# Optimization experiments

Measured on AMD Instinct MI355X. Metric: run time of the kernel, lower is better.

The kernel has to match this reference:

```python
import jax, jax.numpy as jnp
import numpy as np

NS, NV, NB, L = 64, 32, 8, 4      # scalar channels, vector channels, bessel bases, layers
EMB = 32                           # atom-type embedding dim
MAX_R = 3.0                        # cutoff radius
NUM_NEIGH = 32.0                   # avg degree used for scatter normalization
N, E = 10000, 320000
NW = NS * 2 + NV * 2               # per-edge tensor-product weights from radial MLP
MAX_TYPES = 10


def smooth_cutoff(x):
    # e3nn md-example smooth_cutoff: 1 for x<0.5, 0 for x>1, cosine blend between
    u = 2.0 * (x - 1.0)
    y = (1.0 - jnp.cos(jnp.pi * u)) * 0.5
    y = jnp.where(u > 0.0, 0.0, y)
    y = jnp.where(u < -1.0, 1.0, y)
    return y


def bessel_basis(r):
    # soft_one_hot_linspace(basis='bessel', cutoff=False) * sqrt(NB)
    n = jnp.arange(1, NB + 1, dtype=r.dtype)
    y = jnp.sqrt(2.0 / MAX_R) * jnp.sin(n * jnp.pi * r[:, None] / MAX_R) / r[:, None]
    return y * np.sqrt(NB).astype(np.float32)


def edge_info(x, src, dst):
    feats, attrs = [], []
    for i in range(2):  # nvec = x.shape[-1] // 3 = 2
        vec = x[src, 3 * i:3 * i + 3] - x[dst, 3 * i:3 * i + 3]  # [E,3]
        r = jnp.linalg.norm(vec, axis=1)
        sh = np.float32(np.sqrt(3.0)) * vec / r[:, None]          # 1x1o SH, component norm
        feats.append(bessel_basis(r))
        attrs.append(smooth_cutoff(r / MAX_R)[:, None] * sh)
    return jnp.concatenate(feats, axis=-1), jnp.stack(attrs, axis=1)  # [E,2*NB], [E,2,3]


def _forward(x, emb_table, W_up, W_proj, fc1, b1, fc2, W_sv, W_vs, W_sc_s, W_sc_v, Ws, Wv, h, mix, node_attr, edge_src, edge_dst):
    n = x.shape[0]
    inv_nb = np.float32(1.0 / np.sqrt(NUM_NEIGH))
    # uplift: 2 input vectors -> NV hidden vectors, NS hidden scalars (zero init)
    xv = x.reshape(n, 2, 3)
    v = jnp.einsum('nic,iv->nvc', xv, W_up)        # [n,NV,3]
    s = jnp.zeros((n, NS), x.dtype)                # [n,NS]
    s_old, v_old = s, v
    attr_emb = emb_table[node_attr]                # [n,EMB]
    xcur = x
    for i in range(L):
        f, a = edge_info(xcur, edge_src, edge_dst)            # [E,2NB], [E,2,3]
        w = jax.nn.silu(f @ fc1[i] + b1[i]) @ fc2[i]          # [E,NW] radial TP weights
        w1 = w[:, :NS * 2].reshape(-1, NS, 2)                 # 0e x 1o -> 1o path weights
        w2 = w[:, NS * 2:].reshape(-1, NV, 2)                 # 1o x 1o -> 0e path weights
        # equivariant tensor-product messages (gather at edge_src)
        t = s[edge_src][:, :, None] * w1                      # [E,NS,2]
        q = jnp.einsum('euv,uvm->evm', t, W_sv[i])            # [E,2,NV]
        msg_v = jnp.einsum('evm,evc->emc', q, a)              # [E,NV,3]
        d = jnp.einsum('euc,evc->euv', v[edge_src], a)        # [E,NV,2]
        msg_s = jnp.einsum('euv,uvm->em', d * w2, W_vs[i])    # [E,NS+NV]
        # scatter-add at edge_dst, normalized by sqrt(num_neighbors)
        agg_s = jnp.zeros((n, NS + NV), x.dtype).at[edge_dst].add(msg_s) * inv_nb
        agg_v = jnp.zeros((n, NV, 3), x.dtype).at[edge_dst].add(msg_v) * inv_nb
        # self-connection: fully-connected TP with node-attr scalars
        sc_s = jnp.einsum('nu,ne,uem->nm', s, attr_emb, W_sc_s[i])
        sc_v = jnp.einsum('nuc,ne,uev->nvc', v, attr_emb, W_sc_v[i])
        cs = sc_s + agg_s
        cv = sc_v + agg_v
        # Gate: silu on scalars, sigmoid gate scalars modulate vectors
        gs = jax.nn.silu(cs[:, :NS])
        gate = jax.nn.sigmoid(cs[:, NS:])
        gv = cv * gate[:, :, None]
        # self-interaction (equivariant linear per degree)
        si_s = s @ Ws[i]
        si_v = jnp.einsum('nuc,uv->nvc', v, Wv[i])
        # verlet-like update
        hi2 = h[i] ** 2
        s_new = 2.0 * s - s_old + hi2 * (mix[i] * gs + (mix[i] - 1.0) * si_s)
        v_new = 2.0 * v - v_old + hi2 * (mix[i] * gv + (mix[i] - 1.0) * si_v)
        s_old, v_old = s, v
        s, v = s_new, v_new
        # project back to x for next layer's edge features
        xcur = jnp.einsum('nvc,vi->nic', v, W_proj).reshape(n, 6)
    return xcur


def setup_inputs() -> dict:
    key = jax.random.key(0)
    ks = jax.random.split(key, 20)
    x = jax.random.normal(ks[0], (N, 6), jnp.float32)
    node_attr = jax.random.randint(ks[1], (N,), 0, MAX_TYPES)
    edge_src = jax.random.randint(ks[2], (E,), 0, N)
    off = jax.random.randint(ks[3], (E,), 1, N)
    edge_dst = (edge_src + off) % N  # no self-loops -> no zero edge_vec
    batch = jnp.zeros((N,), jnp.int32)
    rn = lambda k, sh, sc: jax.random.normal(k, sh, jnp.float32) * np.float32(sc)
    emb_table = rn(ks[4], (MAX_TYPES, EMB), 0.5)
    W_up = rn(ks[5], (2, NV), 1.0 / np.sqrt(2))
    W_proj = rn(ks[6], (NV, 2), 1.0 / np.sqrt(NV))
    fc1 = rn(ks[7], (L, 2 * NB, 64), 1.0 / np.sqrt(2 * NB))
    b1 = jnp.zeros((L, 64), jnp.float32)
    fc2 = rn(ks[8], (L, 64, NW), 1.0 / np.sqrt(64))
    W_sv = rn(ks[9], (L, NS, 2, NV), 1.0 / np.sqrt(NS * 2))
    W_vs = rn(ks[10], (L, NV, 2, NS + NV), 1.0 / np.sqrt(NV * 2))
    W_sc_s = rn(ks[11], (L, NS, EMB, NS + NV), 1.0 / np.sqrt(NS * EMB))
    W_sc_v = rn(ks[12], (L, NV, EMB, NV), 1.0 / np.sqrt(NV * EMB))
    Ws = rn(ks[13], (L, NS, NS), 1.0 / np.sqrt(NS))
    Wv = rn(ks[14], (L, NV, NV), 1.0 / np.sqrt(NV))
    h = jnp.ones((L,), jnp.float32) * 0.01
    mix = jnp.ones((L,), jnp.float32) * 0.5
    return {"x": x, "emb_table": emb_table, "W_up": W_up, "W_proj": W_proj, "fc1": fc1, "b1": b1, "fc2": fc2, "W_sv": W_sv, "W_vs": W_vs, "W_sc_s": W_sc_s, "W_sc_v": W_sc_v, "Ws": Ws, "Wv": Wv, "h": h, "mix": mix, "node_attr": node_attr, "edge_src": edge_src, "edge_dst": edge_dst, "batch": batch}


def reference(x, emb_table, W_up, W_proj, fc1, b1, fc2, W_sv, W_vs, W_sc_s, W_sc_v, Ws, Wv, h, mix, node_attr, edge_src, edge_dst, batch):
    return _forward(x, emb_table, W_up, W_proj, fc1, b1, fc2, W_sv, W_vs, W_sc_s, W_sc_v, Ws, Wv, h, mix, node_attr, edge_src, edge_dst)
```

## Files before the change

### kernel.cpp

```cpp
#include <hip/hip_runtime.h>
#include <math.h>

constexpr int cNS = 64, cNV = 32, cNB = 8, cL = 4, cEMB = 32, cNT = 10;
constexpr float PI_F = 3.14159265358979323846f;
constexpr float INV_SQRT_NN = 0.17677669529663687f;
constexpr float BESSEL_C = 2.3094010767585034f;
constexpr float SQRT3 = 1.7320508075688772f;

typedef unsigned short u16;
typedef unsigned int u32;
typedef unsigned long long u64;
typedef __attribute__((ext_vector_type(8))) short bf16x8;
typedef __attribute__((ext_vector_type(4))) float f32x4;
typedef __attribute__((ext_vector_type(2))) float f32x2;
typedef __attribute__((ext_vector_type(4))) int i32x4;

__device__ __forceinline__ u16 f2b(float x) {
  u32 u = __float_as_uint(x);
  return (u16)((u + 0x7fffu + ((u >> 16) & 1u)) >> 16);
}
__device__ __forceinline__ float b2f(u16 h) { return __uint_as_float(((u32)h) << 16); }
__device__ __forceinline__ float blo(u32 w) { return __uint_as_float(w << 16); }
__device__ __forceinline__ float bhi(u32 w) { return __uint_as_float(w & 0xffff0000u); }

__device__ __forceinline__ u32 pkbf(float lo, float hi) {
  u32 r;
  asm("v_cvt_pk_bf16_f32 %0, %1, %2" : "=v"(r) : "v"(lo), "v"(hi));
  return r;
}

__device__ __forceinline__ void lds_fence() {
  asm volatile("s_waitcnt lgkmcnt(0)" ::: "memory");
  __builtin_amdgcn_sched_barrier(0);
}

union U8 { bf16x8 v; u32 w[4]; };

__device__ __forceinline__ f32x4 mfma16(bf16x8 a, bf16x8 b, f32x4 c) {
  return __builtin_amdgcn_mfma_f32_16x16x32_bf16(a, b, c, 0, 0, 0);
}


__global__ void k_precompA(const float* __restrict__ emb, const float* __restrict__ Wss,
                           float* __restrict__ A) {
  int idx = blockIdx.x * 256 + threadIdx.x;
  if (idx >= cL * cNT * 64 * 96) return;
  int m = idx % 96;
  int u = (idx / 96) % 64;
  int t = (idx / (96 * 64)) % cNT;
  int l = idx / (96 * 64 * cNT);
  float acc = 0.f;
#pragma unroll
  for (int e = 0; e < 32; ++e)
    acc += emb[t * 32 + e] * Wss[((size_t)(l * 64 + u) * 32 + e) * 96 + m];
  A[idx] = acc;
}

__global__ void k_precompB(const float* __restrict__ emb, const float* __restrict__ Wsv_,
                           float* __restrict__ B) {
  int idx = blockIdx.x * 256 + threadIdx.x;
  if (idx >= cL * cNT * 32 * 32) return;
  int vo = idx % 32;
  int u = (idx / 32) % 32;
  int t = (idx / 1024) % cNT;
  int l = idx / (1024 * cNT);
  float acc = 0.f;
#pragma unroll
  for (int e = 0; e < 32; ++e)
    acc += emb[t * 32 + e] * Wsv_[((size_t)(l * 32 + u) * 32 + e) * 32 + vo];
  B[idx] = acc;
}

__global__ void k_packB(const float* __restrict__ fc2, const float* __restrict__ Wsv,
                        const float* __restrict__ Wvs, const float* __restrict__ fc1,
                        u16* __restrict__ fc2L, u16* __restrict__ WsvL,
                        u16* __restrict__ WvsL, u16* __restrict__ fc1L) {
  int idx = blockIdx.x * 256 + threadIdx.x;
  const int T1 = cL * 12288, T2 = cL * 2 * 2048, T3 = cL * 2 * 3072, T4 = cL * 2048;
  if (idx < T1) {
    int l = idx / 12288, r = idx % 12288;
    int ki = r & 7, tt = r >> 3;
    int nn = tt % 192, kq = tt / 192;
    fc2L[idx] = f2b(fc2[((size_t)(l * 64) + kq * 8 + ki) * 192 + nn]);
  } else if (idx < T1 + T2) {
    int r0 = idx - T1;
    int l = r0 / 4096, r1 = r0 % 4096;
    int k2 = r1 / 2048, r = r1 % 2048;
    int ki = r & 7, tt = r >> 3;
    int mm = tt % 32, kq = tt / 32;
    WsvL[r0] = f2b(Wsv[((size_t)((l * 64 + kq * 8 + ki) * 2) + k2) * 32 + mm]);
  } else if (idx < T1 + T2 + T3) {
    int r0 = idx - T1 - T2;
    int l = r0 / 6144, r1 = r0 % 6144;
    int k2 = r1 / 3072, r = r1 % 3072;
    int ki = r & 7, tt = r >> 3;
    int mm = tt % 96, kq = tt / 96;
    WvsL[r0] = f2b(Wvs[((size_t)((l * 32 + kq * 8 + ki) * 2) + k2) * 96 + mm]);
  } else if (idx < T1 + T2 + T3 + T4) {
    int r0 = idx - T1 - T2 - T3;
    int l = r0 / 2048, r1 = r0 % 2048;
    int kq = r1 / 512, rem = r1 % 512;
    int n = rem / 8, ki = rem & 7;
    fc1L[r0] = (kq < 2) ? f2b(fc1[l * 1024 + (kq * 8 + ki) * 64 + n]) : (u16)0;
  }
}

__global__ void k_init(const float* __restrict__ x, const float* __restrict__ Wup,
                       float* __restrict__ v, float* __restrict__ v_old,
                       float* __restrict__ xcur, int N) {
  int idx = blockIdx.x * 256 + threadIdx.x;
  if (idx >= N * 32) return;
  int n = idx >> 5, vc = idx & 31;
  float w0 = Wup[vc], w1 = Wup[32 + vc];
#pragma unroll
  for (int c = 0; c < 3; ++c) {
    float val = x[n * 6 + c] * w0 + x[n * 6 + 3 + c] * w1;
    v[idx * 3 + c] = val;
    v_old[idx * 3 + c] = val;
  }
  if (vc < 6) xcur[n * 6 + vc] = x[n * 6 + vc];
}


__global__ void k_zero_i(int* __restrict__ p, int n) {
  int i = blockIdx.x * 256 + threadIdx.x;
  if (i < n) p[i] = 0;
}

__global__ void k_hist(const int* __restrict__ edst, int* __restrict__ deg, int E) {
  int e = blockIdx.x * 256 + threadIdx.x;
  if (e < E) atomicAdd(&deg[edst[e]], 1);
}

__global__ __launch_bounds__(1024) void k_scan(const int* __restrict__ deg,
                                               int* __restrict__ row_ptr,
                                               int* __restrict__ cursor, int N) {
  __shared__ int part[1024];
  int t = threadIdx.x;
  int chunk = (N + 1023) / 1024;
  int base = t * chunk;
  int sum = 0;
  for (int i = 0; i < chunk; ++i) {
    int idx = base + i;
    if (idx < N) sum += deg[idx];
  }
  part[t] = sum;
  __syncthreads();
  for (int off = 1; off < 1024; off <<= 1) {
    int val = (t >= off) ? part[t - off] : 0;
    __syncthreads();
    part[t] += val;
    __syncthreads();
  }
  int run = (t > 0) ? part[t - 1] : 0;
  for (int i = 0; i < chunk; ++i) {
    int idx = base + i;
    if (idx < N) {
      row_ptr[idx] = run;
      cursor[idx] = run;
      run += deg[idx];
    }
  }
  if (t == 1023) row_ptr[N] = part[1023];
}

__global__ void k_scatter(const int* __restrict__ esrc, const int* __restrict__ edst,
                          int* __restrict__ cursor, int* __restrict__ esrc_s,
                          int* __restrict__ edst_s, int E) {
  int e = blockIdx.x * 256 + threadIdx.x;
  if (e < E) {
    int d = edst[e];
    int p = atomicAdd(&cursor[d], 1);
    esrc_s[p] = esrc[e];
    edst_s[p] = d;
  }
}

template <bool SZERO>
__global__ __launch_bounds__(256) void k_edge_mfma(
    const float* __restrict__ xcur, const float* __restrict__ s, const float* __restrict__ v,
    const int* __restrict__ esrc_s, const int* __restrict__ edst_s,
    const u16* __restrict__ fc1L, const float* __restrict__ b1,
    const u16* __restrict__ fc2L, const u16* __restrict__ WsvL0,
    const u16* __restrict__ WsvL1, const u16* __restrict__ WvsL0,
    const u16* __restrict__ WvsL1, u16* __restrict__ msgbuf, int E) {
  __shared__ u16 wbAll[4][16 * 200];
  __shared__ float aAll[4][16][6];
  int wid = threadIdx.x >> 6, lane = threadIdx.x & 63;
  int e0 = (blockIdx.x * 4 + wid) * 16;
  if (e0 >= E) return;
  u16* wb = wbAll[wid];
  int lrow = lane & 15, lg = lane >> 4;

  int prow = e0 + lrow;
  if (prow >= E) prow = E - 1;
  int src = esrc_s[prow];

  {
    int el = lane >> 2, qq = lane & 3;
    int ge = e0 + el;
    if (ge >= E) ge = E - 1;
    int gs = esrc_s[ge], gd = edst_s[ge];
    float xs[6], xd[6];
    {
      const float2* ps = (const float2*)(xcur + (size_t)gs * 6);
      const float2* pd = (const float2*)(xcur + (size_t)gd * 6);
      float2 A0 = ps[0], A1 = ps[1], A2 = ps[2];
      float2 B0 = pd[0], B1 = pd[1], B2 = pd[2];
      xs[0] = A0.x; xs[1] = A0.y; xs[2] = A1.x; xs[3] = A1.y; xs[4] = A2.x; xs[5] = A2.y;
      xd[0] = B0.x; xd[1] = B0.y; xd[2] = B1.x; xd[3] = B1.y; xd[4] = B2.x; xd[5] = B2.y;
    }
    float f[16], av[6];
#pragma unroll
    for (int i = 0; i < 2; ++i) {
      float vx = xs[3 * i + 0] - xd[3 * i + 0];
      float vy = xs[3 * i + 1] - xd[3 * i + 1];
      float vz = xs[3 * i + 2] - xd[3 * i + 2];
      float r2 = vx * vx + vy * vy + vz * vz;
      float rr = sqrtf(r2);
      float invr = 1.0f / rr;
      float th = (PI_F / 3.0f) * rr;
      float s1, c1;
      __sincosf(th, &s1, &c1);
      float twc = 2.0f * c1;
      float snm = 0.f, sn = s1;
      float fc = BESSEL_C * invr;
#pragma unroll
      for (int nn = 0; nn < 8; ++nn) {
        f[8 * i + nn] = fc * sn;
        float nx = twc * sn - snm;
        snm = sn;
        sn = nx;
      }
      float uu = (2.0f / 3.0f) * rr - 2.0f;
      float cut;
      if (uu > 0.f) cut = 0.f;
      else if (uu < -1.f) cut = 1.f;
      else cut = (1.0f - __cosf(PI_F * uu)) * 0.5f;
      float sc = cut * SQRT3 * invr;
      av[3 * i + 0] = vx * sc; av[3 * i + 1] = vy * sc; av[3 * i + 2] = vz * sc;
    }
    if (qq == 0) {
      u32* fp = (u32*)(wb + 1600 + el * 40);
#pragma unroll
      for (int i = 0; i < 8; ++i) fp[i] = pkbf(f[2 * i], f[2 * i + 1]);
#pragma unroll
      for (int i = 8; i < 16; ++i) fp[i] = 0u;
      float* ap = aAll[wid][el];
#pragma unroll
      for (int i = 0; i < 6; ++i) ap[i] = av[i];
    }
  }

  float sv0[8], sv1[8], vl[24];
  if (!SZERO) {
    const float* sp = s + (size_t)src * 64;
    *(f32x4*)(sv0) = *(const f32x4*)(sp + lg * 8);
    *(f32x4*)(sv0 + 4) = *(const f32x4*)(sp + lg * 8 + 4);
    *(f32x4*)(sv1) = *(const f32x4*)(sp + 32 + lg * 8);
    *(f32x4*)(sv1 + 4) = *(const f32x4*)(sp + 32 + lg * 8 + 4);
  }
  {
    const float* vp = v + (size_t)src * 96 + lg * 24;
#pragma unroll
    for (int i = 0; i < 6; ++i) *(f32x4*)(vl + 4 * i) = *(const f32x4*)(vp + 4 * i);
  }

  lds_fence();

  {
    bf16x8 fA = *(const bf16x8*)(wb + 1600 + lrow * 40 + lg * 8);
    f32x4 hp[4];
#pragma unroll
    for (int nb = 0; nb < 4; ++nb) {
      bf16x8 bB = *(const bf16x8*)(fc1L + (size_t)(lg * 64 + nb * 16 + lrow) * 8);
      f32x4 z = {0.f, 0.f, 0.f, 0.f};
      hp[nb] = mfma16(fA, bB, z);
    }
#pragma unroll
    for (int nb = 0; nb < 4; ++nb) {
      float bias = b1[nb * 16 + lrow];
      float hv[4];
#pragma unroll
      for (int r = 0; r < 4; ++r) {
        float xv = hp[nb][r] + bias;
        hv[r] = xv * (1.0f / (1.0f + __expf(-xv)));
      }
      u32 p01 = pkbf(hv[0], hv[1]);
      u32 p23 = pkbf(hv[2], hv[3]);
      int col = nb * 16 + lrow;
      wb[(4 * lg + 0) * 72 + col] = (u16)p01;
      wb[(4 * lg + 1) * 72 + col] = (u16)(p01 >> 16);
      wb[(4 * lg + 2) * 72 + col] = (u16)p23;
      wb[(4 * lg + 3) * 72 + col] = (u16)(p23 >> 16);
    }
  }
  lds_fence();

  bf16x8 ha = *(const bf16x8*)(wb + lrow * 72 + lg * 8);
  bf16x8 hbf = *(const bf16x8*)(wb + lrow * 72 + 32 + lg * 8);
  lds_fence();

  int xw = lg << 3;
#pragma unroll
  for (int nb = (SZERO ? 8 : 0); nb < 12; ++nb) {
    bf16x8 b0 = *(const bf16x8*)(fc2L + (size_t)(lg * 192 + nb * 16 + lrow) * 8);
    bf16x8 b1v = *(const bf16x8*)(fc2L + (size_t)((4 + lg) * 192 + nb * 16 + lrow) * 8);
    f32x4 c = {0.f, 0.f, 0.f, 0.f};
    c = mfma16(ha, b0, c);
    c = mfma16(hbf, b1v, c);
    int n = nb * 16 + lrow;
    int pn = (n < 128) ? ((n & 1) * 64 + (n >> 1)) : (128 + (n & 1) * 32 + ((n - 128) >> 1));
    int rbase = 4 * lg * 200 + (pn ^ xw);
    u32 p01 = pkbf(c[0], c[1]);
    u32 p23 = pkbf(c[2], c[3]);
    wb[rbase] = (u16)p01;
    wb[rbase + 200] = (u16)(p01 >> 16);
    wb[rbase + 400] = (u16)p23;
    wb[rbase + 600] = (u16)(p23 >> 16);
  }
  lds_fence();

  const u16* wrow = wb + lrow * 200 + (((lg ^ (lrow >> 2)) & 3) << 3);

  f32x4 q0[2], q1[2];
  if (!SZERO) {
    i32x4 W0a = *(const i32x4*)(wrow);
    i32x4 W0b = *(const i32x4*)(wrow + 32);
    i32x4 W1a = *(const i32x4*)(wrow + 64);
    i32x4 W1b = *(const i32x4*)(wrow + 96);
    U8 t0a, t0b, t1a, t1b;
#pragma unroll
    for (int j2 = 0; j2 < 4; ++j2) {
      u32 wa = (u32)W0a[j2], wbv = (u32)W0b[j2], wc = (u32)W1a[j2], wd = (u32)W1b[j2];
      t0a.w[j2] = pkbf(sv0[2 * j2] * blo(wa), sv0[2 * j2 + 1] * bhi(wa));
      t0b.w[j2] = pkbf(sv1[2 * j2] * blo(wbv), sv1[2 * j2 + 1] * bhi(wbv));
      t1a.w[j2] = pkbf(sv0[2 * j2] * blo(wc), sv0[2 * j2 + 1] * bhi(wc));
      t1b.w[j2] = pkbf(sv1[2 * j2] * blo(wd), sv1[2 * j2 + 1] * bhi(wd));
    }
#pragma unroll
    for (int nb = 0; nb < 2; ++nb) {
      bf16x8 bA = *(const bf16x8*)(WsvL0 + (size_t)(lg * 32 + nb * 16 + lrow) * 8);
      bf16x8 bB = *(const bf16x8*)(WsvL0 + (size_t)((4 + lg) * 32 + nb * 16 + lrow) * 8);
      f32x4 c = {0.f, 0.f, 0.f, 0.f};
      c = mfma16(t0a.v, bA, c);
      c = mfma16(t0b.v, bB, c);
      q0[nb] = c;
      bf16x8 bC = *(const bf16x8*)(WsvL1 + (size_t)(lg * 32 + nb * 16 + lrow) * 8);
      bf16x8 bD = *(const bf16x8*)(WsvL1 + (size_t)((4 + lg) * 32 + nb * 16 + lrow) * 8);
      f32x4 c2 = {0.f, 0.f, 0.f, 0.f};
      c2 = mfma16(t1a.v, bC, c2);
      c2 = mfma16(t1b.v, bD, c2);
      q1[nb] = c2;
    }
  }

  float a00, a01, a02, a10, a11, a12;
  {
    const float* ap = aAll[wid][lrow];
    a00 = ap[0]; a01 = ap[1]; a02 = ap[2]; a10 = ap[3]; a11 = ap[4]; a12 = ap[5];
  }
  i32x4 W2a = *(const i32x4*)(wrow + 128);
  i32x4 W2b = *(const i32x4*)(wrow + 160);
  U8 ga, gb;
#pragma unroll
  for (int j2 = 0; j2 < 4; ++j2) {
    float d0a, d1a, d0b, d1b;
    {
      float vx = vl[6 * j2 + 0], vy = vl[6 * j2 + 1], vz = vl[6 * j2 + 2];
      d0a = vx * a00 + vy * a01 + vz * a02;
      d1a = vx * a10 + vy * a11 + vz * a12;
    }
    {
      float vx = vl[6 * j2 + 3], vy = vl[6 * j2 + 4], vz = vl[6 * j2 + 5];
      d0b = vx * a00 + vy * a01 + vz * a02;
      d1b = vx * a10 + vy * a11 + vz * a12;
    }
    u32 wa = (u32)W2a[j2], wbv = (u32)W2b[j2];
    ga.w[j2] = pkbf(d0a * blo(wa), d0b * bhi(wa));
    gb.w[j2] = pkbf(d1a * blo(wbv), d1b * bhi(wbv));
  }
  f32x4 mS[6];
#pragma unroll
  for (int nb = 0; nb < 6; ++nb) {
    bf16x8 b0 = *(const bf16x8*)(WvsL0 + (size_t)(lg * 96 + nb * 16 + lrow) * 8);
    bf16x8 b1v = *(const bf16x8*)(WvsL1 + (size_t)(lg * 96 + nb * 16 + lrow) * 8);
    f32x4 c = {0.f, 0.f, 0.f, 0.f};
    c = mfma16(ga.v, b0, c);
    c = mfma16(gb.v, b1v, c);
    mS[nb] = c;
  }

  lds_fence();
#pragma unroll
  for (int nb = 0; nb < 6; ++nb) {
    u32 p01 = pkbf(mS[nb][0], mS[nb][1]);
    u32 p23 = pkbf(mS[nb][2], mS[nb][3]);
    int colx = (nb * 16 + lrow) ^ xw;
    wb[(4 * lg + 0) * 200 + colx] = (u16)p01;
    wb[(4 * lg + 1) * 200 + colx] = (u16)(p01 >> 16);
    wb[(4 * lg + 2) * 200 + colx] = (u16)p23;
    wb[(4 * lg + 3) * 200 + colx] = (u16)(p23 >> 16);
  }
  if (!SZERO) {
#pragma unroll
    for (int nb = 0; nb < 2; ++nb) {
#pragma unroll
      for (int r = 0; r < 4; ++r) {
        int el = 4 * lg + r;
        const float* ap = aAll[wid][el];
        float Q0v = q0[nb][r], Q1v = q1[nb][r];
        float v0 = Q0v * ap[0] + Q1v * ap[3];
        float v1 = Q0v * ap[1] + Q1v * ap[4];
        float v2 = Q0v * ap[2] + Q1v * ap[5];
        u32 p01 = pkbf(v0, v1);
        int base = el * 200 + ((96 + nb * 16 + lrow) ^ xw);
        wb[base] = (u16)p01;
        wb[base + 32] = (u16)(p01 >> 16);
        wb[base + 64] = f2b(v2);
      }
    }
  }
  lds_fence();

  int orow = lane >> 2, oq = lane & 3;
  if (e0 + orow < E) {
    const int OST = SZERO ? 96 : 192;
    u16* gdst = msgbuf + (size_t)(e0 + orow) * OST;
    int xo = ((orow >> 2) & 3) << 3;
    const int NIT = SZERO ? 3 : 6;
#pragma unroll
    for (int it = 0; it < NIT; ++it) {
      int col = oq * 8 + it * 32;
      i32x4 d = *(const i32x4*)(wb + orow * 200 + (col ^ xo));
      *(i32x4*)(gdst + col) = d;
    }
  }
}

template <bool SZERO>
__global__ __launch_bounds__(256) void k_gnode(
    const u16* __restrict__ msg, const int* __restrict__ row_ptr,
    float* __restrict__ s, float* __restrict__ sold, float* __restrict__ v,
    float* __restrict__ vold,
    const float* __restrict__ Amat, const float* __restrict__ Bmat,
    const float* __restrict__ Ws, const float* __restrict__ Wv,
    const float* __restrict__ Wproj, const int* __restrict__ nattr,
    const float* __restrict__ hArr, const float* __restrict__ mixArr, int layer,
    float* __restrict__ xout, int N) {
  int half = threadIdx.x >> 7;
  int t = threadIdx.x & 127;
  int n = blockIdx.x * 2 + half;
  bool active = n < N;
  if (!active) n = N - 1;
  __shared__ float agg[2][192];
  __shared__ float srow[2][64];
  __shared__ float vrow[2][96];
  __shared__ float gateS[2][32];
  __shared__ float vnewS[2][96];
  int start = row_ptr[n], end = row_ptr[n + 1];
  const int STRIDE = SZERO ? 96 : 192;
  int nacc4 = SZERO ? 24 : 48;
  if (t < nacc4) {
    const u16* mp = msg + (size_t)t * 4;
    float accA[4] = {0.f, 0.f, 0.f, 0.f};
    float accB[4] = {0.f, 0.f, 0.f, 0.f};
    int p = start;
    for (; p + 8 <= end; p += 8) {
      u64 w[8];
#pragma unroll
      for (int k = 0; k < 8; ++k) w[k] = *(const u64*)(mp + (size_t)(p + k) * STRIDE);
#pragma unroll
      for (int k = 0; k < 8; ++k) {
        u32 wl = (u32)w[k], wh = (u32)(w[k] >> 32);
        float* acc = (k & 1) ? accB : accA;
        acc[0] += blo(wl);
        acc[1] += bhi(wl);
        acc[2] += blo(wh);
        acc[3] += bhi(wh);
      }
    }
    for (; p < end; ++p) {
      u64 w = *(const u64*)(mp + (size_t)p * STRIDE);
      u32 wl = (u32)w, wh = (u32)(w >> 32);
      accA[0] += blo(wl);
      accA[1] += bhi(wl);
      accA[2] += blo(wh);
      accA[3] += bhi(wh);
    }
#pragma unroll
    for (int c = 0; c < 4; ++c)
      agg[half][4 * t + c] = (accA[c] + accB[c]) * INV_SQRT_NN;
  }
  if (SZERO && t >= 24 && t < 48) {
#pragma unroll
    for (int c = 0; c < 4; ++c) agg[half][4 * t + c] = 0.f;
  }
  if (t < 64) srow[half][t] = s[(size_t)n * 64 + t];
  if (t < 96) vrow[half][t] = v[(size_t)n * 96 + t];
  __syncthreads();
  int type = nattr[n];
  float hv = hArr[layer];
  float h2v = hv * hv;
  float mx = mixArr[layer];
  float cs = 0.f;
  if (t < 96) {
    cs = agg[half][t];
    const float* Ac = Amat + (size_t)type * 64 * 96 + t;
#pragma unroll 8
    for (int u = 0; u < 64; ++u) cs += srow[half][u] * Ac[u * 96];
  }
  if (t >= 64 && t < 96) gateS[half][t - 64] = 1.0f / (1.0f + __expf(-cs));
  __syncthreads();
  if (t < 64) {
    float gs = cs * (1.0f / (1.0f + __expf(-cs)));
    float sis = 0.f;
#pragma unroll 8
    for (int u = 0; u < 64; ++u) sis += srow[half][u] * Ws[u * 64 + t];
    float scur = srow[half][t];
    float sprev = sold[(size_t)n * 64 + t];
    float snew = 2.f * scur - sprev + h2v * (mx * gs + (mx - 1.f) * sis);
    if (active) {
      sold[(size_t)n * 64 + t] = scur;
      s[(size_t)n * 64 + t] = snew;
    }
  }
  if (t < 96) {
    int vch = t / 3, c = t - vch * 3;
    float cv = agg[half][96 + c * 32 + vch];
    const float* Bc = Bmat + (size_t)type * 1024 + vch;
    float scv = 0.f, siv = 0.f;
#pragma unroll 8
    for (int u = 0; u < 32; ++u) {
      float vu = vrow[half][u * 3 + c];
      scv += vu * Bc[u * 32];
      siv += vu * Wv[u * 32 + vch];
    }
    cv += scv;
    float gv = cv * gateS[half][vch];
    float vcur = vrow[half][t];
    float vprev = vold[(size_t)n * 96 + t];
    float vnew = 2.f * vcur - vprev + h2v * (mx * gv + (mx - 1.f) * siv);
    if (active) {
      vold[(size_t)n * 96 + t] = vcur;
      v[(size_t)n * 96 + t] = vnew;
    }
    vnewS[half][t] = vnew;
  }
  __syncthreads();
  if (t < 6 && active) {
    int i = t / 3, c = t - i * 3;
    float acc = 0.f;
#pragma unroll
    for (int vo = 0; vo < 32; ++vo) acc += vnewS[half][vo * 3 + c] * Wproj[vo * 2 + i];
    xout[(size_t)n * 6 + t] = acc;
  }
}

extern "C" void kernel_launch(void* const* d_in, const int* in_sizes, int n_in,
                              void* d_out, int out_size, void* d_ws, size_t ws_size,
                              hipStream_t stream) {
  const float* x = (const float*)d_in[0];
  const float* emb = (const float*)d_in[1];
  const float* Wup = (const float*)d_in[2];
  const float* Wproj = (const float*)d_in[3];
  const float* fc1 = (const float*)d_in[4];
  const float* b1 = (const float*)d_in[5];
  const float* fc2 = (const float*)d_in[6];
  const float* Wsv = (const float*)d_in[7];
  const float* Wvs = (const float*)d_in[8];
  const float* Wscs = (const float*)d_in[9];
  const float* Wscv = (const float*)d_in[10];
  const float* Ws = (const float*)d_in[11];
  const float* Wv = (const float*)d_in[12];
  const float* hArr = (const float*)d_in[13];
  const float* mixArr = (const float*)d_in[14];
  const int* nattr = (const int*)d_in[15];
  const int* esrc = (const int*)d_in[16];
  const int* edst = (const int*)d_in[17];

  const int N = in_sizes[0] / 6;
  const int E = in_sizes[16];

  float* ws = (float*)d_ws;
  size_t off = 0;
  auto alloc = [&](size_t nf) {
    float* p = ws + off;
    off += (nf + 3) & ~(size_t)3;
    return p;
  };
  float* sbuf = alloc((size_t)N * 64);
  float* sold = alloc((size_t)N * 64);
  float* vbuf = alloc((size_t)N * 96);
  float* vold = alloc((size_t)N * 96);
  float* xcur = alloc((size_t)N * 6);
  float* Amat = alloc((size_t)cL * cNT * 64 * 96);
  float* Bmat = alloc((size_t)cL * cNT * 32 * 32);
  u16* fc2L = (u16*)alloc((size_t)cL * 6144);
  u16* WsvL = (u16*)alloc((size_t)cL * 2048);
  u16* WvsL = (u16*)alloc((size_t)cL * 3072);
  u16* fc1L = (u16*)alloc((size_t)cL * 1024);
  int* deg = (int*)alloc((size_t)(N + 4));
  int* row_ptr = (int*)alloc((size_t)(N + 4));
  int* cursor = (int*)alloc((size_t)(N + 4));
  int* esrc_s = (int*)alloc((size_t)E);
  int* edst_s = (int*)alloc((size_t)E);
  u16* msgbuf = (u16*)alloc((size_t)E * 96);

  hipMemsetAsync(sbuf, 0, sizeof(float) * (size_t)N * 128, stream);
  k_init<<<(N * 32 + 255) / 256, 256, 0, stream>>>(x, Wup, vbuf, vold, xcur, N);
  k_precompA<<<(cL * cNT * 64 * 96 + 255) / 256, 256, 0, stream>>>(emb, Wscs, Amat);
  k_precompB<<<(cL * cNT * 32 * 32 + 255) / 256, 256, 0, stream>>>(emb, Wscv, Bmat);
  {
    int tot = cL * 12288 + cL * 4096 + cL * 6144 + cL * 2048;
    k_packB<<<(tot + 255) / 256, 256, 0, stream>>>(fc2, Wsv, Wvs, fc1, fc2L, WsvL, WvsL, fc1L);
  }
  k_zero_i<<<(N + 255) / 256, 256, 0, stream>>>(deg, N);
  k_hist<<<(E + 255) / 256, 256, 0, stream>>>(edst, deg, E);
  k_scan<<<1, 1024, 0, stream>>>(deg, row_ptr, cursor, N);
  k_scatter<<<(E + 255) / 256, 256, 0, stream>>>(esrc, edst, cursor, esrc_s, edst_s, E);

  int eblocks = ((E + 15) / 16 + 3) / 4;
  int gblocks = (N + 1) / 2;
  for (int l = 0; l < cL; ++l) {
    if (l == 0)
      k_edge_mfma<true><<<eblocks, 256, 0, stream>>>(
          xcur, sbuf, vbuf, esrc_s, edst_s, fc1L + l * 2048, b1 + l * 64,
          fc2L + l * 12288, WsvL + l * 4096, WsvL + l * 4096 + 2048,
          WvsL + l * 6144, WvsL + l * 6144 + 3072, msgbuf, E);
    else
      k_edge_mfma<false><<<eblocks, 256, 0, stream>>>(
          xcur, sbuf, vbuf, esrc_s, edst_s, fc1L + l * 2048, b1 + l * 64,
          fc2L + l * 12288, WsvL + l * 4096, WsvL + l * 4096 + 2048,
          WvsL + l * 6144, WvsL + l * 6144 + 3072, msgbuf, E);
    float* xout = (l == cL - 1) ? (float*)d_out : xcur;
    if (l == 0)
      k_gnode<true><<<gblocks, 256, 0, stream>>>(
          msgbuf, row_ptr, sbuf, sold, vbuf, vold, Amat + (size_t)l * cNT * 64 * 96,
          Bmat + (size_t)l * cNT * 1024, Ws + l * 4096, Wv + l * 1024, Wproj, nattr,
          hArr, mixArr, l, xout, N);
    else
      k_gnode<false><<<gblocks, 256, 0, stream>>>(
          msgbuf, row_ptr, sbuf, sold, vbuf, vold, Amat + (size_t)l * cNT * 64 * 96,
          Bmat + (size_t)l * cNT * 1024, Ws + l * 4096, Wv + l * 1024, Wproj, nattr,
          hArr, mixArr, l, xout, N);
  }
}
```

Baseline: 559.1 us.

## Process 32 edges per wavefront to reuse weight B-fragments across two MFMA tiles

Each wavefront now handles two 16-edge tiles instead of one. The fc1, fc2, Wsv and Wvs B-fragments loaded from global memory are reused for both tiles, which halves weight-fetch traffic per edge and gives more independent MFMAs to interleave. The edge geometry computation is split across two lanes per edge (one per input vector), and blocks shrink to 128 threads with a larger per-wave LDS buffer. The cost is higher register pressure and LDS use per wave, which may reduce occupancy.

```diff
diff --git a/kernel.cpp b/kernel.cpp
--- a/kernel.cpp
+++ b/kernel.cpp
@@ -177,128 +177,117 @@
 }
 
 template <bool SZERO>
-__global__ __launch_bounds__(256) void k_edge_mfma(
+__global__ __launch_bounds__(128) void k_edge_mfma(
     const float* __restrict__ xcur, const float* __restrict__ s, const float* __restrict__ v,
     const int* __restrict__ esrc_s, const int* __restrict__ edst_s,
     const u16* __restrict__ fc1L, const float* __restrict__ b1,
     const u16* __restrict__ fc2L, const u16* __restrict__ WsvL0,
     const u16* __restrict__ WsvL1, const u16* __restrict__ WvsL0,
     const u16* __restrict__ WvsL1, u16* __restrict__ msgbuf, int E) {
-  __shared__ u16 wbAll[4][16 * 200];
-  __shared__ float aAll[4][16][6];
+  __shared__ u16 wbAll[2][32 * 200];
+  __shared__ float aAll[2][32][6];
   int wid = threadIdx.x >> 6, lane = threadIdx.x & 63;
-  int e0 = (blockIdx.x * 4 + wid) * 16;
+  int e0 = (blockIdx.x * 2 + wid) * 32;
   if (e0 >= E) return;
   u16* wb = wbAll[wid];
   int lrow = lane & 15, lg = lane >> 4;
 
-  int prow = e0 + lrow;
-  if (prow >= E) prow = E - 1;
-  int src = esrc_s[prow];
-
   {
-    int el = lane >> 2, qq = lane & 3;
+    int el = lane >> 1, qq = lane & 1;
     int ge = e0 + el;
     if (ge >= E) ge = E - 1;
     int gs = esrc_s[ge], gd = edst_s[ge];
-    float xs[6], xd[6];
-    {
-      const float2* ps = (const float2*)(xcur + (size_t)gs * 6);
-      const float2* pd = (const float2*)(xcur + (size_t)gd * 6);
-      float2 A0 = ps[0], A1 = ps[1], A2 = ps[2];
-      float2 B0 = pd[0], B1 = pd[1], B2 = pd[2];
-      xs[0] = A0.x; xs[1] = A0.y; xs[2] = A1.x; xs[3] = A1.y; xs[4] = A2.x; xs[5] = A2.y;
-      xd[0] = B0.x; xd[1] = B0.y; xd[2] = B1.x; xd[3] = B1.y; xd[4] = B2.x; xd[5] = B2.y;
-    }
-    float f[16], av[6];
-#pragma unroll
-    for (int i = 0; i < 2; ++i) {
-      float vx = xs[3 * i + 0] - xd[3 * i + 0];
-      float vy = xs[3 * i + 1] - xd[3 * i + 1];
-      float vz = xs[3 * i + 2] - xd[3 * i + 2];
-      float r2 = vx * vx + vy * vy + vz * vz;
-      float rr = sqrtf(r2);
-      float invr = 1.0f / rr;
-      float th = (PI_F / 3.0f) * rr;
-      float s1, c1;
-      __sincosf(th, &s1, &c1);
-      float twc = 2.0f * c1;
-      float snm = 0.f, sn = s1;
-      float fc = BESSEL_C * invr;
-#pragma unroll
-      for (int nn = 0; nn < 8; ++nn) {
-        f[8 * i + nn] = fc * sn;
-        float nx = twc * sn - snm;
-        snm = sn;
-        sn = nx;
-      }
-      float uu = (2.0f / 3.0f) * rr - 2.0f;
-      float cut;
-      if (uu > 0.f) cut = 0.f;
-      else if (uu < -1.f) cut = 1.f;
-      else cut = (1.0f - __cosf(PI_F * uu)) * 0.5f;
-      float sc = cut * SQRT3 * invr;
-      av[3 * i + 0] = vx * sc; av[3 * i + 1] = vy * sc; av[3 * i + 2] = vz * sc;
-    }
-    if (qq == 0) {
-      u32* fp = (u32*)(wb + 1600 + el * 40);
-#pragma unroll
-      for (int i = 0; i < 8; ++i) fp[i] = pkbf(f[2 * i], f[2 * i + 1]);
-#pragma unroll
-      for (int i = 8; i < 16; ++i) fp[i] = 0u;
-      float* ap = aAll[wid][el];
-#pragma unroll
-      for (int i = 0; i < 6; ++i) ap[i] = av[i];
-    }
-  }
-
-  float sv0[8], sv1[8], vl[24];
-  if (!SZERO) {
-    const float* sp = s + (size_t)src * 64;
-    *(f32x4*)(sv0) = *(const f32x4*)(sp + lg * 8);
-    *(f32x4*)(sv0 + 4) = *(const f32x4*)(sp + lg * 8 + 4);
-    *(f32x4*)(sv1) = *(const f32x4*)(sp + 32 + lg * 8);
-    *(f32x4*)(sv1 + 4) = *(const f32x4*)(sp + 32 + lg * 8 + 4);
-  }
+    const float* ps = xcur + (size_t)gs * 6 + qq * 3;
+    const float* pd = xcur + (size_t)gd * 6 + qq * 3;
+    float vx = ps[0] - pd[0];
+    float vy = ps[1] - pd[1];
+    float vz = ps[2] - pd[2];
+    float r2 = vx * vx + vy * vy + vz * vz;
+    float rr = sqrtf(r2);
+    float invr = 1.0f / rr;
+    float th = (PI_F / 3.0f) * rr;
+    float s1, c1;
+    __sincosf(th, &s1, &c1);
+    float twc = 2.0f * c1;
+    float snm = 0.f, sn = s1;
+    float fc = BESSEL_C * invr;
+    float f8[8];
+#pragma unroll
+    for (int nn = 0; nn < 8; ++nn) {
+      f8[nn] = fc * sn;
+      float nx = twc * sn - snm;
+      snm = sn;
+      sn = nx;
+    }
+    float uu = (2.0f / 3.0f) * rr - 2.0f;
+    float cut;
+    if (uu > 0.f) cut = 0.f;
+    else if (uu < -1.f) cut = 1.f;
+    else cut = (1.0f - __cosf(PI_F * uu)) * 0.5f;
+    float sc = cut * SQRT3 * invr;
+    u32* fp = (u32*)(wb + 5120 + el * 40);
+#pragma unroll
+    for (int i = 0; i < 4; ++i) fp[qq * 4 + i] = pkbf(f8[2 * i], f8[2 * i + 1]);
+#pragma unroll
+    for (int i = 0; i < 4; ++i) fp[8 + qq * 4 + i] = 0u;
+    float* ap = aAll[wid][el];
+    ap[qq * 3 + 0] = vx * sc;
+    ap[qq * 3 + 1] = vy * sc;
+    ap[qq * 3 + 2] = vz * sc;
+  }
+  lds_fence();
+
   {
-    const float* vp = v + (size_t)src * 96 + lg * 24;
-#pragma unroll
-    for (int i = 0; i < 6; ++i) *(f32x4*)(vl + 4 * i) = *(const f32x4*)(vp + 4 * i);
-  }
-
-  lds_fence();
-
-  {
-    bf16x8 fA = *(const bf16x8*)(wb + 1600 + lrow * 40 + lg * 8);
-    f32x4 hp[4];
+    bf16x8 fA0 = *(const bf16x8*)(wb + 5120 + lrow * 40 + lg * 8);
+    bf16x8 fA1 = *(const bf16x8*)(wb + 5120 + (16 + lrow) * 40 + lg * 8);
+    f32x4 hp0[4], hp1[4];
 #pragma unroll
     for (int nb = 0; nb < 4; ++nb) {
       bf16x8 bB = *(const bf16x8*)(fc1L + (size_t)(lg * 64 + nb * 16 + lrow) * 8);
       f32x4 z = {0.f, 0.f, 0.f, 0.f};
-      hp[nb] = mfma16(fA, bB, z);
+      hp0[nb] = mfma16(fA0, bB, z);
+      hp1[nb] = mfma16(fA1, bB, z);
     }
 #pragma unroll
     for (int nb = 0; nb < 4; ++nb) {
       float bias = b1[nb * 16 + lrow];
-      float hv[4];
-#pragma unroll
-      for (int r = 0; r < 4; ++r) {
-        float xv = hp[nb][r] + bias;
-        hv[r] = xv * (1.0f / (1.0f + __expf(-xv)));
-      }
-      u32 p01 = pkbf(hv[0], hv[1]);
-      u32 p23 = pkbf(hv[2], hv[3]);
       int col = nb * 16 + lrow;
-      wb[(4 * lg + 0) * 72 + col] = (u16)p01;
-      wb[(4 * lg + 1) * 72 + col] = (u16)(p01 >> 16);
-      wb[(4 * lg + 2) * 72 + col] = (u16)p23;
-      wb[(4 * lg + 3) * 72 + col] = (u16)(p23 >> 16);
+      {
+        float hv[4];
+#pragma unroll
+        for (int r = 0; r < 4; ++r) {
+          float xv = hp0[nb][r] + bias;
+          hv[r] = xv * (1.0f / (1.0f + __expf(-xv)));
+        }
+        u32 p01 = pkbf(hv[0], hv[1]);
+        u32 p23 = pkbf(hv[2], hv[3]);
+        wb[(4 * lg + 0) * 72 + col] = (u16)p01;
+        wb[(4 * lg + 1) * 72 + col] = (u16)(p01 >> 16);
+        wb[(4 * lg + 2) * 72 + col] = (u16)p23;
+        wb[(4 * lg + 3) * 72 + col] = (u16)(p23 >> 16);
+      }
+      {
+        float hv[4];
+#pragma unroll
+        for (int r = 0; r < 4; ++r) {
+          float xv = hp1[nb][r] + bias;
+          hv[r] = xv * (1.0f / (1.0f + __expf(-xv)));
+        }
+        u32 p01 = pkbf(hv[0], hv[1]);
+        u32 p23 = pkbf(hv[2], hv[3]);
+        wb[(16 + 4 * lg + 0) * 72 + col] = (u16)p01;
+        wb[(16 + 4 * lg + 1) * 72 + col] = (u16)(p01 >> 16);
+        wb[(16 + 4 * lg + 2) * 72 + col] = (u16)p23;
+        wb[(16 + 4 * lg + 3) * 72 + col] = (u16)(p23 >> 16);
+      }
     }
   }
   lds_fence();
 
-  bf16x8 ha = *(const bf16x8*)(wb + lrow * 72 + lg * 8);
-  bf16x8 hbf = *(const bf16x8*)(wb + lrow * 72 + 32 + lg * 8);
+  bf16x8 ha0 = *(const bf16x8*)(wb + lrow * 72 + lg * 8);
+  bf16x8 hbf0 = *(const bf16x8*)(wb + lrow * 72 + 32 + lg * 8);
+  bf16x8 ha1 = *(const bf16x8*)(wb + (16 + lrow) * 72 + lg * 8);
+  bf16x8 hbf1 = *(const bf16x8*)(wb + (16 + lrow) * 72 + 32 + lg * 8);
   lds_fence();
 
   int xw = lg << 3;
@@ -306,132 +295,177 @@
   for (int nb = (SZERO ? 8 : 0); nb < 12; ++nb) {
     bf16x8 b0 = *(const bf16x8*)(fc2L + (size_t)(lg * 192 + nb * 16 + lrow) * 8);
     bf16x8 b1v = *(const bf16x8*)(fc2L + (size_t)((4 + lg) * 192 + nb * 16 + lrow) * 8);
-    f32x4 c = {0.f, 0.f, 0.f, 0.f};
-    c = mfma16(ha, b0, c);
-    c = mfma16(hbf, b1v, c);
+    f32x4 z = {0.f, 0.f, 0.f, 0.f};
+    f32x4 c0 = mfma16(ha0, b0, z);
+    c0 = mfma16(hbf0, b1v, c0);
+    f32x4 c1 = mfma16(ha1, b0, z);
+    c1 = mfma16(hbf1, b1v, c1);
     int n = nb * 16 + lrow;
     int pn = (n < 128) ? ((n & 1) * 64 + (n >> 1)) : (128 + (n & 1) * 32 + ((n - 128) >> 1));
-    int rbase = 4 * lg * 200 + (pn ^ xw);
-    u32 p01 = pkbf(c[0], c[1]);
-    u32 p23 = pkbf(c[2], c[3]);
-    wb[rbase] = (u16)p01;
-    wb[rbase + 200] = (u16)(p01 >> 16);
-    wb[rbase + 400] = (u16)p23;
-    wb[rbase + 600] = (u16)(p23 >> 16);
+    int cx = pn ^ xw;
+    {
+      int rb = (4 * lg) * 200 + cx;
+      u32 p01 = pkbf(c0[0], c0[1]);
+      u32 p23 = pkbf(c0[2], c0[3]);
+      wb[rb] = (u16)p01;
+      wb[rb + 200] = (u16)(p01 >> 16);
+      wb[rb + 400] = (u16)p23;
+      wb[rb + 600] = (u16)(p23 >> 16);
+    }
+    {
+      int rb = (16 + 4 * lg) * 200 + cx;
+      u32 p01 = pkbf(c1[0], c1[1]);
+      u32 p23 = pkbf(c1[2], c1[3]);
+      wb[rb] = (u16)p01;
+      wb[rb + 200] = (u16)(p01 >> 16);
+      wb[rb + 400] = (u16)p23;
+      wb[rb + 600] = (u16)(p23 >> 16);
+    }
   }
   lds_fence();
 
-  const u16* wrow = wb + lrow * 200 + (((lg ^ (lrow >> 2)) & 3) << 3);
-
-  f32x4 q0[2], q1[2];
+  const u16* wrow0 = wb + lrow * 200 + (((lg ^ (lrow >> 2)) & 3) << 3);
+  const u16* wrow1 = wrow0 + 3200;
+
+  int prow0 = e0 + lrow;
+  if (prow0 >= E) prow0 = E - 1;
+  int prow1 = e0 + 16 + lrow;
+  if (prow1 >= E) prow1 = E - 1;
+  int srcs[2] = {esrc_s[prow0], esrc_s[prow1]};
+
+  f32x4 q0[2][2], q1[2][2];
   if (!SZERO) {
-    i32x4 W0a = *(const i32x4*)(wrow);
-    i32x4 W0b = *(const i32x4*)(wrow + 32);
-    i32x4 W1a = *(const i32x4*)(wrow + 64);
-    i32x4 W1b = *(const i32x4*)(wrow + 96);
-    U8 t0a, t0b, t1a, t1b;
-#pragma unroll
-    for (int j2 = 0; j2 < 4; ++j2) {
-      u32 wa = (u32)W0a[j2], wbv = (u32)W0b[j2], wc = (u32)W1a[j2], wd = (u32)W1b[j2];
-      t0a.w[j2] = pkbf(sv0[2 * j2] * blo(wa), sv0[2 * j2 + 1] * bhi(wa));
-      t0b.w[j2] = pkbf(sv1[2 * j2] * blo(wbv), sv1[2 * j2 + 1] * bhi(wbv));
-      t1a.w[j2] = pkbf(sv0[2 * j2] * blo(wc), sv0[2 * j2 + 1] * bhi(wc));
-      t1b.w[j2] = pkbf(sv1[2 * j2] * blo(wd), sv1[2 * j2 + 1] * bhi(wd));
+    U8 t0a[2], t0b[2], t1a[2], t1b[2];
+#pragma unroll
+    for (int h = 0; h < 2; ++h) {
+      const u16* wr = h ? wrow1 : wrow0;
+      const float* sp = s + (size_t)srcs[h] * 64;
+      float sv0[8], sv1[8];
+      *(f32x4*)(sv0) = *(const f32x4*)(sp + lg * 8);
+      *(f32x4*)(sv0 + 4) = *(const f32x4*)(sp + lg * 8 + 4);
+      *(f32x4*)(sv1) = *(const f32x4*)(sp + 32 + lg * 8);
+      *(f32x4*)(sv1 + 4) = *(const f32x4*)(sp + 32 + lg * 8 + 4);
+      i32x4 W0a = *(const i32x4*)(wr);
+      i32x4 W0b = *(const i32x4*)(wr + 32);
+      i32x4 W1a = *(const i32x4*)(wr + 64);
+      i32x4 W1b = *(const i32x4*)(wr + 96);
+#pragma unroll
+      for (int j2 = 0; j2 < 4; ++j2) {
+        u32 wa = (u32)W0a[j2], wbv = (u32)W0b[j2], wc = (u32)W1a[j2], wd = (u32)W1b[j2];
+        t0a[h].w[j2] = pkbf(sv0[2 * j2] * blo(wa), sv0[2 * j2 + 1] * bhi(wa));
+        t0b[h].w[j2] = pkbf(sv1[2 * j2] * blo(wbv), sv1[2 * j2 + 1] * bhi(wbv));
+        t1a[h].w[j2] = pkbf(sv0[2 * j2] * blo(wc), sv0[2 * j2 + 1] * bhi(wc));
+        t1b[h].w[j2] = pkbf(sv1[2 * j2] * blo(wd), sv1[2 * j2 + 1] * bhi(wd));
+      }
     }
 #pragma unroll
     for (int nb = 0; nb < 2; ++nb) {
       bf16x8 bA = *(const bf16x8*)(WsvL0 + (size_t)(lg * 32 + nb * 16 + lrow) * 8);
       bf16x8 bB = *(const bf16x8*)(WsvL0 + (size_t)((4 + lg) * 32 + nb * 16 + lrow) * 8);
-      f32x4 c = {0.f, 0.f, 0.f, 0.f};
-      c = mfma16(t0a.v, bA, c);
-      c = mfma16(t0b.v, bB, c);
-      q0[nb] = c;
       bf16x8 bC = *(const bf16x8*)(WsvL1 + (size_t)(lg * 32 + nb * 16 + lrow) * 8);
       bf16x8 bD = *(const bf16x8*)(WsvL1 + (size_t)((4 + lg) * 32 + nb * 16 + lrow) * 8);
-      f32x4 c2 = {0.f, 0.f, 0.f, 0.f};
-      c2 = mfma16(t1a.v, bC, c2);
-      c2 = mfma16(t1b.v, bD, c2);
-      q1[nb] = c2;
-    }
-  }
-
-  float a00, a01, a02, a10, a11, a12;
-  {
-    const float* ap = aAll[wid][lrow];
-    a00 = ap[0]; a01 = ap[1]; a02 = ap[2]; a10 = ap[3]; a11 = ap[4]; a12 = ap[5];
-  }
-  i32x4 W2a = *(const i32x4*)(wrow + 128);
-  i32x4 W2b = *(const i32x4*)(wrow + 160);
-  U8 ga, gb;
-#pragma unroll
-  for (int j2 = 0; j2 < 4; ++j2) {
-    float d0a, d1a, d0b, d1b;
-    {
-      float vx = vl[6 * j2 + 0], vy = vl[6 * j2 + 1], vz = vl[6 * j2 + 2];
-      d0a = vx * a00 + vy * a01 + vz * a02;
-      d1a = vx * a10 + vy * a11 + vz * a12;
-    }
-    {
-      float vx = vl[6 * j2 + 3], vy = vl[6 * j2 + 4], vz = vl[6 * j2 + 5];
-      d0b = vx * a00 + vy * a01 + vz * a02;
-      d1b = vx * a10 + vy * a11 + vz * a12;
-    }
-    u32 wa = (u32)W2a[j2], wbv = (u32)W2b[j2];
-    ga.w[j2] = pkbf(d0a * blo(wa), d0b * bhi(wa));
-    gb.w[j2] = pkbf(d1a * blo(wbv), d1b * bhi(wbv));
-  }
-  f32x4 mS[6];
+#pragma unroll
+      for (int h = 0; h < 2; ++h) {
+        f32x4 z = {0.f, 0.f, 0.f, 0.f};
+        f32x4 c = mfma16(t0a[h].v, bA, z);
+        c = mfma16(t0b[h].v, bB, c);
+        q0[h][nb] = c;
+        f32x4 c2 = mfma16(t1a[h].v, bC, z);
+        c2 = mfma16(t1b[h].v, bD, c2);
+        q1[h][nb] = c2;
+      }
+    }
+  }
+
+  U8 ga[2], gb[2];
+#pragma unroll
+  for (int h = 0; h < 2; ++h) {
+    const float* ap = aAll[wid][h * 16 + lrow];
+    float a00 = ap[0], a01 = ap[1], a02 = ap[2], a10 = ap[3], a11 = ap[4], a12 = ap[5];
+    float vl[24];
+    const float* vp = v + (size_t)srcs[h] * 96 + lg * 24;
+#pragma unroll
+    for (int i = 0; i < 6; ++i) *(f32x4*)(vl + 4 * i) = *(const f32x4*)(vp + 4 * i);
+    const u16* wr = h ? wrow1 : wrow0;
+    i32x4 W2a = *(const i32x4*)(wr + 128);
+    i32x4 W2b = *(const i32x4*)(wr + 160);
+#pragma unroll
+    for (int j2 = 0; j2 < 4; ++j2) {
+      float d0a, d1a, d0b, d1b;
+      {
+        float vx = vl[6 * j2 + 0], vy = vl[6 * j2 + 1], vz = vl[6 * j2 + 2];
+        d0a = vx * a00 + vy * a01 + vz * a02;
+        d1a = vx * a10 + vy * a11 + vz * a12;
+      }
+      {
+        float vx = vl[6 * j2 + 3], vy = vl[6 * j2 + 4], vz = vl[6 * j2 + 5];
+        d0b = vx * a00 + vy * a01 + vz * a02;
+        d1b = vx * a10 + vy * a11 + vz * a12;
+      }
+      u32 wa = (u32)W2a[j2], wbv = (u32)W2b[j2];
+      ga[h].w[j2] = pkbf(d0a * blo(wa), d0b * bhi(wa));
+      gb[h].w[j2] = pkbf(d1a * blo(wbv), d1b * bhi(wbv));
+    }
+  }
+  f32x4 mS[2][6];
 #pragma unroll
   for (int nb = 0; nb < 6; ++nb) {
     bf16x8 b0 = *(const bf16x8*)(WvsL0 + (size_t)(lg * 96 + nb * 16 + lrow) * 8);
     bf16x8 b1v = *(const bf16x8*)(WvsL1 + (size_t)(lg * 96 + nb * 16 + lrow) * 8);
-    f32x4 c = {0.f, 0.f, 0.f, 0.f};
-    c = mfma16(ga.v, b0, c);
-    c = mfma16(gb.v, b1v, c);
-    mS[nb] = c;
+#pragma unroll
+    for (int h = 0; h < 2; ++h) {
+      f32x4 z = {0.f, 0.f, 0.f, 0.f};
+      f32x4 c = mfma16(ga[h].v, b0, z);
+      c = mfma16(gb[h].v, b1v, c);
+      mS[h][nb] = c;
+    }
   }
 
   lds_fence();
 #pragma unroll
-  for (int nb = 0; nb < 6; ++nb) {
-    u32 p01 = pkbf(mS[nb][0], mS[nb][1]);
-    u32 p23 = pkbf(mS[nb][2], mS[nb][3]);
-    int colx = (nb * 16 + lrow) ^ xw;
-    wb[(4 * lg + 0) * 200 + colx] = (u16)p01;
-    wb[(4 * lg + 1) * 200 + colx] = (u16)(p01 >> 16);
-    wb[(4 * lg + 2) * 200 + colx] = (u16)p23;
-    wb[(4 * lg + 3) * 200 + colx] = (u16)(p23 >> 16);
-  }
-  if (!SZERO) {
-#pragma unroll
-    for (int nb = 0; nb < 2; ++nb) {
-#pragma unroll
-      for (int r = 0; r < 4; ++r) {
-        int el = 4 * lg + r;
-        const float* ap = aAll[wid][el];
-        float Q0v = q0[nb][r], Q1v = q1[nb][r];
-        float v0 = Q0v * ap[0] + Q1v * ap[3];
-        float v1 = Q0v * ap[1] + Q1v * ap[4];
-        float v2 = Q0v * ap[2] + Q1v * ap[5];
-        u32 p01 = pkbf(v0, v1);
-        int base = el * 200 + ((96 + nb * 16 + lrow) ^ xw);
-        wb[base] = (u16)p01;
-        wb[base + 32] = (u16)(p01 >> 16);
-        wb[base + 64] = f2b(v2);
+  for (int h = 0; h < 2; ++h) {
+    int rbase = (h * 16 + 4 * lg) * 200;
+#pragma unroll
+    for (int nb = 0; nb < 6; ++nb) {
+      u32 p01 = pkbf(mS[h][nb][0], mS[h][nb][1]);
+      u32 p23 = pkbf(mS[h][nb][2], mS[h][nb][3]);
+      int colx = (nb * 16 + lrow) ^ xw;
+      wb[rbase + colx] = (u16)p01;
+      wb[rbase + 200 + colx] = (u16)(p01 >> 16);
+      wb[rbase + 400 + colx] = (u16)p23;
+      wb[rbase + 600 + colx] = (u16)(p23 >> 16);
+    }
+    if (!SZERO) {
+#pragma unroll
+      for (int nb = 0; nb < 2; ++nb) {
+#pragma unroll
+        for (int r = 0; r < 4; ++r) {
+          int el = h * 16 + 4 * lg + r;
+          const float* ap = aAll[wid][el];
+          float Q0v = q0[h][nb][r], Q1v = q1[h][nb][r];
+          float v0 = Q0v * ap[0] + Q1v * ap[3];
+          float v1 = Q0v * ap[1] + Q1v * ap[4];
+          float v2 = Q0v * ap[2] + Q1v * ap[5];
+          u32 p01 = pkbf(v0, v1);
+          int base = el * 200 + ((96 + nb * 16 + lrow) ^ xw);
+          wb[base] = (u16)p01;
+          wb[base + 32] = (u16)(p01 >> 16);
+          wb[base + 64] = f2b(v2);
+        }
       }
     }
   }
   lds_fence();
 
-  int orow = lane >> 2, oq = lane & 3;
+  int orow = lane >> 1, oq = lane & 1;
   if (e0 + orow < E) {
     const int OST = SZERO ? 96 : 192;
     u16* gdst = msgbuf + (size_t)(e0 + orow) * OST;
     int xo = ((orow >> 2) & 3) << 3;
-    const int NIT = SZERO ? 3 : 6;
+    const int NIT = SZERO ? 6 : 12;
 #pragma unroll
     for (int it = 0; it < NIT; ++it) {
-      int col = oq * 8 + it * 32;
+      int col = oq * 8 + it * 16;
       i32x4 d = *(const i32x4*)(wb + orow * 200 + (col ^ xo));
       *(i32x4*)(gdst + col) = d;
     }
@@ -620,16 +654,16 @@
   k_scan<<<1, 1024, 0, stream>>>(deg, row_ptr, cursor, N);
   k_scatter<<<(E + 255) / 256, 256, 0, stream>>>(esrc, edst, cursor, esrc_s, edst_s, E);
 
-  int eblocks = ((E + 15) / 16 + 3) / 4;
+  int eblocks = (E + 63) / 64;
   int gblocks = (N + 1) / 2;
   for (int l = 0; l < cL; ++l) {
     if (l == 0)
-      k_edge_mfma<true><<<eblocks, 256, 0, stream>>>(
+      k_edge_mfma<true><<<eblocks, 128, 0, stream>>>(
           xcur, sbuf, vbuf, esrc_s, edst_s, fc1L + l * 2048, b1 + l * 64,
           fc2L + l * 12288, WsvL + l * 4096, WsvL + l * 4096 + 2048,
           WvsL + l * 6144, WvsL + l * 6144 + 3072, msgbuf, E);
     else
-      k_edge_mfma<false><<<eblocks, 256, 0, stream>>>(
+      k_edge_mfma<false><<<eblocks, 128, 0, stream>>>(
           xcur, sbuf, vbuf, esrc_s, edst_s, fc1L + l * 2048, b1 + l * 64,
           fc2L + l * 12288, WsvL + l * 4096, WsvL + l * 4096 + 2048,
           WvsL + l * 6144, WvsL + l * 6144 + 3072, msgbuf, E);
```

Measured after the change: 556.9 us. Within noise of the previous version (-0.4%).
